# Kernel tuning notes

Hardware: AMD Instinct MI355X
Metric: run time of the kernel (lower is better)

## Reference

```python
import jax, jax.numpy as jnp
import numpy as np

N, E, B, L = 32768, 524288, 64, 512  # nodes, edges, graphs, max nodes/graph
V, D, H = 10000, 256, 512            # vocab, embed_dim, hidden_dim


def gcn_conv(h, W, b, src, dst, n):
    """PyG GCNConv: add self-loops, symmetric deg normalization, scatter-sum."""
    h = h @ W  # [n, out]
    loops = jnp.arange(n)
    s = jnp.concatenate([src, loops])
    d = jnp.concatenate([dst, loops])
    deg = jax.ops.segment_sum(jnp.ones_like(d, dtype=h.dtype), d, num_segments=n)
    dinv = jnp.where(deg > 0, jax.lax.rsqrt(deg), 0.0)
    norm = dinv[s] * dinv[d]  # [E+n]
    out = jax.ops.segment_sum(h[s] * norm[:, None], d, num_segments=n)
    return out + b


def gru_seq(x, Wih, Whh, bih, bhh):
    """torch nn.GRU (1 layer, batch_first). x: [B, T, H] -> outputs [T, B, H]."""
    def step(h, x_t):
        gi = x_t @ Wih.T + bih          # [B, 3H]
        gh = h @ Whh.T + bhh            # [B, 3H]
        ir, iz, inn = jnp.split(gi, 3, axis=-1)
        hr, hz, hn = jnp.split(gh, 3, axis=-1)
        r = jax.nn.sigmoid(ir + hr)
        z = jax.nn.sigmoid(iz + hz)
        n = jnp.tanh(inn + r * hn)
        h = (1.0 - z) * n + z * h
        return h, h
    h0 = jnp.zeros((x.shape[0], Whh.shape[1]), x.dtype)
    _, outs = jax.lax.scan(step, h0, jnp.swapaxes(x, 0, 1))
    return outs  # [T, B, H]


def setup_inputs() -> dict:
    key = jax.random.key(0)
    ks = jax.random.split(key, 16)
    s = 0.05
    x = jax.random.randint(ks[0], (N,), 0, V)
    edge_index = jax.random.randint(ks[1], (2, E), 0, N)
    batch_idx = jnp.arange(N) // L  # sorted graph ids, L nodes per graph
    focal_points = jax.random.uniform(ks[2], (B, 1), jnp.float32)
    return {
        "x": x, "edge_index": edge_index, "batch_idx": batch_idx,
        "focal_points": focal_points,
        "emb": jax.random.normal(ks[3], (V, D), jnp.float32) * s,
        "W1": jax.random.normal(ks[4], (D, H), jnp.float32) * s,
        "b1": jnp.zeros((H,), jnp.float32),
        "W2": jax.random.normal(ks[5], (H, H), jnp.float32) * s,
        "b2": jnp.zeros((H,), jnp.float32),
        "Wih": jax.random.normal(ks[6], (3 * H, H), jnp.float32) * s,
        "Whh": jax.random.normal(ks[7], (3 * H, H), jnp.float32) * s,
        "bih": jnp.zeros((3 * H,), jnp.float32),
        "bhh": jnp.zeros((3 * H,), jnp.float32),
        "fc1_w": jax.random.normal(ks[8], (H + 1, H), jnp.float32) * s,
        "fc1_b": jnp.zeros((H,), jnp.float32),
        "fc2_w": jax.random.normal(ks[9], (H, 1), jnp.float32) * s,
        "fc2_b": jnp.zeros((1,), jnp.float32),
    }


def reference(x, edge_index, batch_idx, focal_points, emb, W1, b1, W2, b2,
              Wih, Whh, bih, bhh, fc1_w, fc1_b, fc2_w, fc2_b):
    src, dst = edge_index[0], edge_index[1]
    h = emb[x]  # [N, D]
    h = jax.nn.relu(gcn_conv(h, W1, b1, src, dst, N))
    h = jax.nn.relu(gcn_conv(h, W2, b2, src, dst, N))  # [N, H]

    # Ragged -> padded: scatter each node to (graph, position-within-graph)
    ones = jnp.ones((N,), h.dtype)
    counts = jax.ops.segment_sum(ones, batch_idx, num_segments=B)
    starts = jnp.cumsum(counts) - counts  # exclusive cumsum
    pos = jnp.arange(N) - starts[batch_idx].astype(jnp.int32)
    padded = jnp.zeros((B, L, H), h.dtype).at[batch_idx, pos].set(h)

    gru_out = gru_seq(padded, Wih, Whh, bih, bhh)   # [L, B, H]
    graph_emb = gru_out.mean(axis=0)                # [B, H]
    g = jnp.concatenate([graph_emb, focal_points], axis=1)  # [B, H+1]
    out = jax.nn.relu(g @ fc1_w + fc1_b)
    out = jax.nn.sigmoid(out @ fc2_w + fc2_b)       # [B, 1]
    return out
```

## Files before the change

kernel.cpp:

```cpp
#include <hip/hip_runtime.h>

#define NODES 32768
#define EDGES 524288
#define BGR   64
#define LSEQ  512
#define DEMB  256
#define HDIM  512

typedef unsigned short u16;
typedef unsigned int   u32;
typedef unsigned long long u64;
typedef __attribute__((ext_vector_type(8))) short short8;
typedef __attribute__((ext_vector_type(4))) float f32x4;

__device__ __forceinline__ float bf2f(u16 u){ u32 x = ((u32)u)<<16; float f; __builtin_memcpy(&f,&x,4); return f; }
__device__ __forceinline__ u16 f2bf(float f){ u32 x; __builtin_memcpy(&x,&f,4); u32 r = x + 0x7fffu + ((x>>16)&1u); return (u16)(r>>16); }
__device__ __forceinline__ float lo16(u32 u){ u32 x = u<<16; float f; __builtin_memcpy(&f,&x,4); return f; }
__device__ __forceinline__ float hi16(u32 u){ u32 x = u & 0xffff0000u; float f; __builtin_memcpy(&f,&x,4); return f; }
__device__ __forceinline__ u32 pack2(float a, float b){ return (u32)f2bf(a) | ((u32)f2bf(b)<<16); }


__global__ void zero_i32(int* p, int n){
  int i = blockIdx.x*256 + threadIdx.x;
  if (i < n) p[i] = 0;
}

__global__ void transpose_cast(const float* __restrict__ in, u16* __restrict__ out, int K, int N){
  int i = blockIdx.x*256 + threadIdx.x;
  if (i < N*K){ int n = i / K, k = i - n*K; out[i] = f2bf(in[(size_t)k*N + n]); }
}

__global__ void cast_bf(const float* __restrict__ in, u16* __restrict__ out, int n){
  int i = blockIdx.x*256 + threadIdx.x;
  if (i < n) out[i] = f2bf(in[i]);
}

__global__ void count_indeg(const int* __restrict__ dst, int* __restrict__ indeg){
  int e = blockIdx.x*256 + threadIdx.x;
  if (e < EDGES) atomicAdd(&indeg[dst[e]], 1);
}

__global__ void compute_dinv(const int* __restrict__ indeg, float* __restrict__ dinv){
  int i = blockIdx.x*256 + threadIdx.x;
  if (i < NODES) dinv[i] = rsqrtf((float)(indeg[i] + 1));
}

__global__ __launch_bounds__(1024) void scan_csr(const int* __restrict__ indeg,
                                                 int* __restrict__ row_ptr,
                                                 int* __restrict__ cursor){
  __shared__ int part[1024];
  int tid = threadIdx.x, base = tid*32;
  int loc[32]; int s = 0;
  for (int i=0;i<32;i++){ loc[i] = s; s += indeg[base+i]; }
  part[tid] = s; __syncthreads();
  for (int off=1; off<1024; off<<=1){
    int v = part[tid]; int add = (tid>=off) ? part[tid-off] : 0;
    __syncthreads(); part[tid] = v + add; __syncthreads();
  }
  int offt = (tid==0) ? 0 : part[tid-1];
  for (int i=0;i<32;i++){ int v = offt + loc[i]; row_ptr[base+i] = v; cursor[base+i] = v; }
}

__global__ void fill_csr(const int* __restrict__ src, const int* __restrict__ dst,
                         int* __restrict__ cursor, int* __restrict__ csr_src){
  int e = blockIdx.x*256 + threadIdx.x;
  if (e < EDGES){ int d = dst[e]; int p = atomicAdd(&cursor[d], 1); csr_src[p] = src[e]; }
}

__global__ __launch_bounds__(256) void agg_emb(const int* __restrict__ x, const u16* __restrict__ embb,
    const float* __restrict__ dinv, const int* __restrict__ row_ptr, const int* __restrict__ indeg,
    const int* __restrict__ csr_src, u16* __restrict__ out){
  int node = blockIdx.x*4 + (threadIdx.x>>6);
  int lane = threadIdx.x & 63;
  float di = dinv[node];
  int xi = x[node];
  u64 hv = *(const u64*)(embb + (size_t)xi*DEMB + lane*4);
  u32 h0 = (u32)hv, h1 = (u32)(hv>>32);
  float a0 = lo16(h0)*di, a1 = hi16(h0)*di, a2 = lo16(h1)*di, a3 = hi16(h1)*di;
  int st = row_ptr[node], cn = indeg[node];
  for (int p = st; p < st+cn; p++){
    int s = csr_src[p];
    float ws = dinv[s];
    u64 v = *(const u64*)(embb + (size_t)x[s]*DEMB + lane*4);
    u32 w0 = (u32)v, w1 = (u32)(v>>32);
    a0 += lo16(w0)*ws; a1 += hi16(w0)*ws; a2 += lo16(w1)*ws; a3 += hi16(w1)*ws;
  }
  u64 pv = (u64)pack2(a0*di,a1*di) | ((u64)pack2(a2*di,a3*di)<<32);
  *(u64*)(out + (size_t)node*DEMB + lane*4) = pv;
}

__global__ __launch_bounds__(256) void agg_h(const u16* __restrict__ hin, const float* __restrict__ dinv,
    const int* __restrict__ row_ptr, const int* __restrict__ indeg,
    const int* __restrict__ csr_src, u16* __restrict__ out){
  int node = blockIdx.x*4 + (threadIdx.x>>6);
  int lane = threadIdx.x & 63;
  float di = dinv[node];
  float a[8];
  uint4 hv = *((const uint4*)(hin + (size_t)node*HDIM) + lane);
  a[0]=lo16(hv.x)*di; a[1]=hi16(hv.x)*di; a[2]=lo16(hv.y)*di; a[3]=hi16(hv.y)*di;
  a[4]=lo16(hv.z)*di; a[5]=hi16(hv.z)*di; a[6]=lo16(hv.w)*di; a[7]=hi16(hv.w)*di;
  int st = row_ptr[node], cn = indeg[node];
  for (int p = st; p < st+cn; p++){
    int s = csr_src[p];
    float ws = dinv[s];
    uint4 v = *((const uint4*)(hin + (size_t)s*HDIM) + lane);
    a[0]+=lo16(v.x)*ws; a[1]+=hi16(v.x)*ws; a[2]+=lo16(v.y)*ws; a[3]+=hi16(v.y)*ws;
    a[4]+=lo16(v.z)*ws; a[5]+=hi16(v.z)*ws; a[6]+=lo16(v.w)*ws; a[7]+=hi16(v.w)*ws;
  }
  uint4 o; o.x=pack2(a[0]*di,a[1]*di); o.y=pack2(a[2]*di,a[3]*di);
  o.z=pack2(a[4]*di,a[5]*di); o.w=pack2(a[6]*di,a[7]*di);
  *(uint4*)(out + (size_t)node*HDIM + lane*8) = o;
}

#define BM 128
#define BN 128
#define BKK 32
__global__ __launch_bounds__(256) void gemm_bt(const u16* __restrict__ A, const u16* __restrict__ BT,
    const float* __restrict__ bias, u16* __restrict__ C, int M, int N, int K, int relu){
  __shared__ u16 aS[BM][BKK+8];
  __shared__ u16 bS[BN][BKK+8];
  int tid = threadIdx.x;
  int m0 = blockIdx.y * BM, n0 = blockIdx.x * BN;
  int lane = tid & 63, w = tid >> 6;
  int wm = w >> 1, wn = w & 1;
  f32x4 acc[4][4];
  for (int i=0;i<4;i++) for (int j=0;j<4;j++) acc[i][j] = (f32x4)0.0f;

  int r  = tid >> 1;
  int cc = (tid & 1) * 16;
  const u16* Ag = A + (size_t)(m0 + r) * K + cc;
  const u16* Bg = BT + (size_t)(n0 + r) * K + cc;
  int l15 = lane & 15, q8 = (lane >> 4) * 8;

  for (int k0 = 0; k0 < K; k0 += BKK) {
    uint4 av0 = *(const uint4*)(Ag + k0);
    uint4 av1 = *(const uint4*)(Ag + k0 + 8);
    uint4 bv0 = *(const uint4*)(Bg + k0);
    uint4 bv1 = *(const uint4*)(Bg + k0 + 8);
    *(uint4*)&aS[r][cc]   = av0; *(uint4*)&aS[r][cc+8] = av1;
    *(uint4*)&bS[r][cc]   = bv0; *(uint4*)&bS[r][cc+8] = bv1;
    __syncthreads();
    short8 af[4], bfr[4];
    for (int i=0;i<4;i++) af[i]  = *(const short8*)&aS[wm*64 + i*16 + l15][q8];
    for (int j=0;j<4;j++) bfr[j] = *(const short8*)&bS[wn*64 + j*16 + l15][q8];
    for (int i=0;i<4;i++)
      for (int j=0;j<4;j++)
        acc[i][j] = __builtin_amdgcn_mfma_f32_16x16x32_bf16(af[i], bfr[j], acc[i][j], 0, 0, 0);
    __syncthreads();
  }
  int q = lane >> 4;
  for (int i=0;i<4;i++) for (int j=0;j<4;j++){
    int col = n0 + wn*64 + j*16 + l15;
    float bval = bias[col];
    for (int rr=0; rr<4; rr++){
      int row = m0 + wm*64 + i*16 + q*4 + rr;
      float v = acc[i][j][rr] + bval;
      if (relu) v = fmaxf(v, 0.f);
      C[(size_t)row * N + col] = f2bf(v);
    }
  }
}

__global__ __launch_bounds__(512) void gru_kernel(const u16* __restrict__ gi,
    const float* __restrict__ Whh, const float* __restrict__ bhh,
    float* __restrict__ graph_emb, u64* __restrict__ xbuf){
  __shared__ __align__(16) u16 w_swz[6*16*65*8];
  __shared__ __align__(16) u16 h_swz[2][16*65*8];
  __shared__ float gh_lds[16*100];

  int tid = threadIdx.x;
  int g = blockIdx.x >> 4, j = blockIdx.x & 15;
  int lane = tid & 63, wave = tid >> 6;
  int l15 = lane & 15, qr = (lane>>4)*4;

  for (int s = tid; s < 6144; s += 512){
    int w = s >> 10, rem = s & 1023, kc = rem >> 6, l = rem & 63;
    int row = l & 15, qq = l >> 4;
    int gate = w >> 1, half = w & 1;
    int c = gate*512 + j*32 + half*16 + row;
    const float* srcp = Whh + (size_t)c*512 + kc*32 + qq*8;
    u16* dst = w_swz + ((size_t)(w*16 + kc)*65 + l)*8;
    #pragma unroll
    for (int i2 = 0; i2 < 8; i2++) dst[i2] = f2bf(srcp[i2]);
  }
  for (int i2 = tid; i2 < 16*65*8; i2 += 512) h_swz[0][i2] = 0;

  int b = tid >> 5, hh = tid & 31;
  int bg = g*16 + b;
  int c_r = j*32 + hh, c_z = 512 + j*32 + hh, c_n = 1024 + j*32 + hh;
  float bias_r = bhh[c_r], bias_z = bhh[c_z], bias_n = bhh[c_n];
  const u16* gi_row = gi + (size_t)bg * LSEQ * 1536;
  float h_prev = 0.f, accm = 0.f;

  u64* xb = xbuf + (size_t)g * 8192;

  u16 gr0 = gi_row[c_r], gz0 = gi_row[c_z], gn0 = gi_row[c_n];
  const u16* gp1 = gi_row + 1536;
  u16 gr1 = gp1[c_r], gz1 = gp1[c_z], gn1 = gp1[c_n];

  int kcc = hh >> 1, qa = (hh & 1) * 2;
  int cb0 = (kcc*65 + (qa  )*16 + b) * 4;
  int cb1 = (kcc*65 + (qa+1)*16 + b) * 4;

  __syncthreads();

  for (int t = 0; t < LSEQ; t++){
    int tn = (t + 2 < LSEQ) ? t + 2 : t;
    const u16* gp2 = gi_row + (size_t)tn * 1536;
    u16 nr = gp2[c_r], nz = gp2[c_z], nn2 = gp2[c_n];

    if (wave < 6){
      const u16* hb = h_swz[t & 1];
      const u16* wb = w_swz + (size_t)wave*16*65*8;
      f32x4 acc0 = (f32x4)0.0f, acc1 = (f32x4)0.0f;
      #pragma unroll
      for (int kc = 0; kc < 8; kc++){
        acc0 = __builtin_amdgcn_mfma_f32_16x16x32_bf16(
                 *(const short8*)(hb + ((size_t)kc*65 + lane)*8),
                 *(const short8*)(wb + ((size_t)kc*65 + lane)*8), acc0, 0, 0, 0);
        acc1 = __builtin_amdgcn_mfma_f32_16x16x32_bf16(
                 *(const short8*)(hb + ((size_t)(kc+8)*65 + lane)*8),
                 *(const short8*)(wb + ((size_t)(kc+8)*65 + lane)*8), acc1, 0, 0, 0);
      }
      f32x4 acc = acc0 + acc1;
      int col = wave*16 + l15;
      #pragma unroll
      for (int rr2 = 0; rr2 < 4; rr2++) gh_lds[(qr + rr2)*100 + col] = acc[rr2];
    }
    __syncthreads();

    float ghr = gh_lds[b*100 + hh]      + bias_r;
    float ghz = gh_lds[b*100 + 32 + hh] + bias_z;
    float ghn = gh_lds[b*100 + 64 + hh] + bias_n;
    float rg = 1.f / (1.f + __expf(-(bf2f(gr0) + ghr)));
    float zg = 1.f / (1.f + __expf(-(bf2f(gz0) + ghz)));
    float pre = bf2f(gn0) + rg * ghn;
    pre = fminf(fmaxf(pre, -20.f), 20.f);
    float e2 = __expf(2.f * pre);
    float nn = (e2 - 1.f) / (e2 + 1.f);
    float h_new = (1.f - zg) * nn + zg * h_prev;
    accm += h_new; h_prev = h_new;

    u32 tag = (u32)(t + 1);
    float h_nb = __shfl_xor(h_new, 1, 64);
    if ((hh & 1) == 0){
      u64 val = ((u64)tag << 32) | (u64)pack2(h_new, h_nb);
      __hip_atomic_store(xb + (size_t)((t&1)*16 + b)*256 + j*16 + (hh>>1), val,
                         __ATOMIC_RELAXED, __HIP_MEMORY_SCOPE_AGENT);
    }

    const u64* rp = xb + (size_t)((t&1)*16 + b)*256 + hh*8;
    u64 v[8];
    bool ok;
    do {
      #pragma unroll
      for (int i=0;i<8;i++) v[i] = __hip_atomic_load(rp + i, __ATOMIC_RELAXED, __HIP_MEMORY_SCOPE_AGENT);
      ok = true;
      #pragma unroll
      for (int i=0;i<8;i++) ok = ok && ((u32)(v[i] >> 32) == tag);
    } while (!ok);

    u32* hl = (u32*)h_swz[(t+1) & 1];
    uint4 w0; w0.x = (u32)v[0]; w0.y = (u32)v[1]; w0.z = (u32)v[2]; w0.w = (u32)v[3];
    uint4 w1; w1.x = (u32)v[4]; w1.y = (u32)v[5]; w1.z = (u32)v[6]; w1.w = (u32)v[7];
    *(uint4*)(hl + cb0) = w0;
    *(uint4*)(hl + cb1) = w1;
    __syncthreads();

    gr0 = gr1; gz0 = gz1; gn0 = gn1;
    gr1 = nr;  gz1 = nz;  gn1 = nn2;
  }
  graph_emb[(size_t)bg*512 + j*32 + hh] = accm * (1.f/512.f);
}

__global__ __launch_bounds__(256) void head(const float* __restrict__ graph_emb, const float* __restrict__ focal,
    const float* __restrict__ fc1w, const float* __restrict__ fc1b,
    const float* __restrict__ fc2w, const float* __restrict__ fc2b, float* __restrict__ out){
  __shared__ float gv[513];
  __shared__ float h1s[512];
  __shared__ float red[4];
  int bq = blockIdx.x, tid = threadIdx.x;
  for (int i = tid; i < 512; i += 256) gv[i] = graph_emb[(size_t)bq*512 + i];
  if (tid == 0) gv[512] = focal[bq];
  __syncthreads();
  for (int c = tid; c < 512; c += 256){
    float acc = fc1b[c];
    for (int k = 0; k < 513; k++) acc += gv[k] * fc1w[(size_t)k*512 + c];
    h1s[c] = fmaxf(acc, 0.f);
  }
  __syncthreads();
  float p = h1s[tid]*fc2w[tid] + h1s[tid+256]*fc2w[tid+256];
  for (int off = 32; off; off >>= 1) p += __shfl_down(p, off, 64);
  if ((tid & 63) == 0) red[tid >> 6] = p;
  __syncthreads();
  if (tid == 0){
    float s = red[0]+red[1]+red[2]+red[3] + fc2b[0];
    out[bq] = 1.f / (1.f + __expf(-s));
  }
}

extern "C" void kernel_launch(void* const* d_in, const int* in_sizes, int n_in,
                              void* d_out, int out_size, void* d_ws, size_t ws_size,
                              hipStream_t stream){
  const int*   x     = (const int*)d_in[0];
  const int*   edge  = (const int*)d_in[1];
  const int*   srcp  = edge;
  const int*   dstp  = edge + EDGES;
  const float* focal = (const float*)d_in[3];
  const float* emb   = (const float*)d_in[4];
  const float* W1    = (const float*)d_in[5];
  const float* b1    = (const float*)d_in[6];
  const float* W2    = (const float*)d_in[7];
  const float* b2    = (const float*)d_in[8];
  const float* Wih   = (const float*)d_in[9];
  const float* Whh   = (const float*)d_in[10];
  const float* bih   = (const float*)d_in[11];
  const float* bhh   = (const float*)d_in[12];
  const float* fc1w  = (const float*)d_in[13];
  const float* fc1b  = (const float*)d_in[14];
  const float* fc2w  = (const float*)d_in[15];
  const float* fc2b  = (const float*)d_in[16];

  char* ws = (char*)d_ws;
  constexpr size_t H2_OFF    = 0;
  constexpr size_t AGG1_OFF  = 33554432;
  constexpr size_t H1_OFF    = 50331648;
  constexpr size_t AGG2_OFF  = 83886080;
  constexpr size_t GI_OFF    = 33554432;
  constexpr size_t MISC      = 134217728;
  constexpr size_t INDEG_OFF = MISC;
  constexpr size_t DINV_OFF  = MISC + 131328;
  constexpr size_t ROWPTR_OFF= MISC + 262400;
  constexpr size_t CURSOR_OFF= MISC + 393472;
  constexpr size_t CSR_OFF   = MISC + 524544;
  constexpr size_t W1T_OFF   = MISC + 2621696;
  constexpr size_t W2T_OFF   = MISC + 2883840;
  constexpr size_t WIHB_OFF  = MISC + 3408128;
  constexpr size_t XBUF_OFF  = MISC + 4980992;
  constexpr size_t GEMB_OFF  = MISC + 5243136;

  int*   indeg  = (int*)(ws + INDEG_OFF);
  float* dinv   = (float*)(ws + DINV_OFF);
  int*   rowptr = (int*)(ws + ROWPTR_OFF);
  int*   cursor = (int*)(ws + CURSOR_OFF);
  int*   csrsrc = (int*)(ws + CSR_OFF);
  u16*   W1T    = (u16*)(ws + W1T_OFF);
  u16*   W2T    = (u16*)(ws + W2T_OFF);
  u16*   WihB   = (u16*)(ws + WIHB_OFF);
  u16*   agg1   = (u16*)(ws + AGG1_OFF);
  u16*   h1     = (u16*)(ws + H1_OFF);
  u16*   agg2   = (u16*)(ws + AGG2_OFF);
  u16*   embb   = (u16*)(ws + AGG2_OFF);
  u16*   h2     = (u16*)(ws + H2_OFF);
  u16*   gi     = (u16*)(ws + GI_OFF);
  u64*   xbuf   = (u64*)(ws + XBUF_OFF);
  float* gemb   = (float*)(ws + GEMB_OFF);

  zero_i32<<<129, 256, 0, stream>>>(indeg, 32768 + 64);
  transpose_cast<<<512, 256, 0, stream>>>(W1, W1T, 256, 512);
  transpose_cast<<<1024, 256, 0, stream>>>(W2, W2T, 512, 512);
  cast_bf<<<3072, 256, 0, stream>>>(Wih, WihB, 1536*512);
  cast_bf<<<10000, 256, 0, stream>>>(emb, embb, 10000*256);
  count_indeg<<<2048, 256, 0, stream>>>(dstp, indeg);
  compute_dinv<<<128, 256, 0, stream>>>(indeg, dinv);
  scan_csr<<<1, 1024, 0, stream>>>(indeg, rowptr, cursor);
  fill_csr<<<2048, 256, 0, stream>>>(srcp, dstp, cursor, csrsrc);
  agg_emb<<<8192, 256, 0, stream>>>(x, embb, dinv, rowptr, indeg, csrsrc, agg1);
  gemm_bt<<<dim3(4, 256), 256, 0, stream>>>(agg1, W1T, b1, h1, NODES, 512, 256, 1);
  agg_h<<<8192, 256, 0, stream>>>(h1, dinv, rowptr, indeg, csrsrc, agg2);
  gemm_bt<<<dim3(4, 256), 256, 0, stream>>>(agg2, W2T, b2, h2, NODES, 512, 512, 1);
  gemm_bt<<<dim3(12, 256), 256, 0, stream>>>(h2, WihB, bih, gi, NODES, 1536, 512, 0);
  gru_kernel<<<64, 512, 0, stream>>>(gi, Whh, bhh, gemb, xbuf);
  head<<<64, 256, 0, stream>>>(gemb, focal, fc1w, fc1b, fc2w, fc2b, (float*)d_out);
}
```

Before: 2.729 ms.

## Replace tagged-payload polling with per-block flag barrier in GRU exchange

The cross-block hidden-state exchange in the GRU kernel used to pack a step tag beside each bf16 pair in 64-bit words, and every thread spun until all eight words it read carried the current tag. Now payloads are plain 32-bit stores. After a vmcnt wait and a block barrier, each block publishes one flag per step, one wave polls the 16 flags of its group, and then all threads read the payload once. This halves exchange traffic and cuts the polling to 16 flags per block instead of every thread. In exchange it adds two extra __syncthreads per step, and it relies on relaxed atomics plus s_waitcnt for ordering, with no explicit release/acquire fence, which may be fragile.

```diff
diff --git a/kernel.cpp b/kernel.cpp
--- a/kernel.cpp
+++ b/kernel.cpp
@@ -163,7 +163,7 @@
 
 __global__ __launch_bounds__(512) void gru_kernel(const u16* __restrict__ gi,
     const float* __restrict__ Whh, const float* __restrict__ bhh,
-    float* __restrict__ graph_emb, u64* __restrict__ xbuf){
+    float* __restrict__ graph_emb, u32* __restrict__ xpay, u32* __restrict__ flg){
   __shared__ __align__(16) u16 w_swz[6*16*65*8];
   __shared__ __align__(16) u16 h_swz[2][16*65*8];
   __shared__ float gh_lds[16*100];
@@ -191,8 +191,6 @@
   float bias_r = bhh[c_r], bias_z = bhh[c_z], bias_n = bhh[c_n];
   const u16* gi_row = gi + (size_t)bg * LSEQ * 1536;
   float h_prev = 0.f, accm = 0.f;
-
-  u64* xb = xbuf + (size_t)g * 8192;
 
   u16 gr0 = gi_row[c_r], gz0 = gi_row[c_z], gn0 = gi_row[c_n];
   const u16* gp1 = gi_row + 1536;
@@ -242,27 +240,40 @@
     accm += h_new; h_prev = h_new;
 
     u32 tag = (u32)(t + 1);
+    int par = t & 1;
+
     float h_nb = __shfl_xor(h_new, 1, 64);
     if ((hh & 1) == 0){
-      u64 val = ((u64)tag << 32) | (u64)pack2(h_new, h_nb);
-      __hip_atomic_store(xb + (size_t)((t&1)*16 + b)*256 + j*16 + (hh>>1), val,
+      u32 pv = pack2(h_new, h_nb);
+      __hip_atomic_store(xpay + (size_t)((g*2 + par)*16 + b)*256 + j*16 + (hh>>1), pv,
                          __ATOMIC_RELAXED, __HIP_MEMORY_SCOPE_AGENT);
     }
-
-    const u64* rp = xb + (size_t)((t&1)*16 + b)*256 + hh*8;
-    u64 v[8];
-    bool ok;
-    do {
-      #pragma unroll
-      for (int i=0;i<8;i++) v[i] = __hip_atomic_load(rp + i, __ATOMIC_RELAXED, __HIP_MEMORY_SCOPE_AGENT);
-      ok = true;
-      #pragma unroll
-      for (int i=0;i<8;i++) ok = ok && ((u32)(v[i] >> 32) == tag);
-    } while (!ok);
+    asm volatile("s_waitcnt vmcnt(0)" ::: "memory");
+    __syncthreads();
+    if (tid == 0)
+      __hip_atomic_store(flg + (g*2 + par)*16 + j, tag,
+                         __ATOMIC_RELAXED, __HIP_MEMORY_SCOPE_AGENT);
+
+    if (tid < 64){
+      const u32* fp = flg + (g*2 + par)*16;
+      bool ok;
+      do {
+        u32 f = (lane < 16)
+              ? __hip_atomic_load(fp + lane, __ATOMIC_RELAXED, __HIP_MEMORY_SCOPE_AGENT)
+              : tag;
+        ok = (f == tag);
+      } while (__ballot(ok) != 0xFFFFFFFFFFFFFFFFull);
+    }
+    __syncthreads();
+
+    const u32* rp = xpay + (size_t)((g*2 + par)*16 + b)*256 + hh*8;
+    u32 v[8];
+    #pragma unroll
+    for (int i=0;i<8;i++) v[i] = __hip_atomic_load(rp + i, __ATOMIC_RELAXED, __HIP_MEMORY_SCOPE_AGENT);
 
     u32* hl = (u32*)h_swz[(t+1) & 1];
-    uint4 w0; w0.x = (u32)v[0]; w0.y = (u32)v[1]; w0.z = (u32)v[2]; w0.w = (u32)v[3];
-    uint4 w1; w1.x = (u32)v[4]; w1.y = (u32)v[5]; w1.z = (u32)v[6]; w1.w = (u32)v[7];
+    uint4 w0; w0.x = v[0]; w0.y = v[1]; w0.z = v[2]; w0.w = v[3];
+    uint4 w1; w1.x = v[4]; w1.y = v[5]; w1.z = v[6]; w1.w = v[7];
     *(uint4*)(hl + cb0) = w0;
     *(uint4*)(hl + cb1) = w1;
     __syncthreads();
@@ -336,7 +347,8 @@
   constexpr size_t W1T_OFF   = MISC + 2621696;
   constexpr size_t W2T_OFF   = MISC + 2883840;
   constexpr size_t WIHB_OFF  = MISC + 3408128;
-  constexpr size_t XBUF_OFF  = MISC + 4980992;
+  constexpr size_t XPAY_OFF  = MISC + 4980992;
+  constexpr size_t FLG_OFF   = MISC + 5112064;
   constexpr size_t GEMB_OFF  = MISC + 5243136;
 
   int*   indeg  = (int*)(ws + INDEG_OFF);
@@ -353,7 +365,8 @@
   u16*   embb   = (u16*)(ws + AGG2_OFF);
   u16*   h2     = (u16*)(ws + H2_OFF);
   u16*   gi     = (u16*)(ws + GI_OFF);
-  u64*   xbuf   = (u64*)(ws + XBUF_OFF);
+  u32*   xpay   = (u32*)(ws + XPAY_OFF);
+  u32*   flg    = (u32*)(ws + FLG_OFF);
   float* gemb   = (float*)(ws + GEMB_OFF);
 
   zero_i32<<<129, 256, 0, stream>>>(indeg, 32768 + 64);
@@ -370,6 +383,6 @@
   agg_h<<<8192, 256, 0, stream>>>(h1, dinv, rowptr, indeg, csrsrc, agg2);
   gemm_bt<<<dim3(4, 256), 256, 0, stream>>>(agg2, W2T, b2, h2, NODES, 512, 512, 1);
   gemm_bt<<<dim3(12, 256), 256, 0, stream>>>(h2, WihB, bih, gi, NODES, 1536, 512, 0);
-  gru_kernel<<<64, 512, 0, stream>>>(gi, Whh, bhh, gemb, xbuf);
+  gru_kernel<<<64, 512, 0, stream>>>(gi, Whh, bhh, gemb, xpay, flg);
   head<<<64, 256, 0, stream>>>(gemb, focal, fc1w, fc1b, fc2w, fc2b, (float*)d_out);
 }
```

Measured after the change: 2.721 ms. No clear change (-0.3%).

## Interleave two graph groups per GRU block to hide cross-block exchange latency

Applied to the files above, without the earlier changes.

Each GRU workgroup now processes two independent 16-graph groups in alternation. Group B's MFMA and gate math run while group A's hidden-state exchange through global memory is in flight, and the reverse. The grid shrinks from 64 to 32 blocks, the gi prefetch-two-steps-ahead is replaced by direct loads each step, and each block does twice the serial work per step. The intent is to hide spin-wait and atomic latency, at the cost of fewer CUs and extra barriers per step.

```diff
diff --git a/kernel.cpp b/kernel.cpp
--- a/kernel.cpp
+++ b/kernel.cpp
@@ -166,10 +166,11 @@
     float* __restrict__ graph_emb, u64* __restrict__ xbuf){
   __shared__ __align__(16) u16 w_swz[6*16*65*8];
   __shared__ __align__(16) u16 h_swz[2][16*65*8];
-  __shared__ float gh_lds[16*100];
+  __shared__ float gh_lds[2][16*100];
 
   int tid = threadIdx.x;
-  int g = blockIdx.x >> 4, j = blockIdx.x & 15;
+  int G2 = blockIdx.x >> 4, j = blockIdx.x & 15;
+  int gA = G2*2, gB = gA + 1;
   int lane = tid & 63, wave = tid >> 6;
   int l15 = lane & 15, qr = (lane>>4)*4;
 
@@ -183,20 +184,16 @@
     #pragma unroll
     for (int i2 = 0; i2 < 8; i2++) dst[i2] = f2bf(srcp[i2]);
   }
-  for (int i2 = tid; i2 < 16*65*8; i2 += 512) h_swz[0][i2] = 0;
+  for (int i2 = tid; i2 < 2*16*65*8; i2 += 512) ((u16*)h_swz)[i2] = 0;
 
   int b = tid >> 5, hh = tid & 31;
-  int bg = g*16 + b;
   int c_r = j*32 + hh, c_z = 512 + j*32 + hh, c_n = 1024 + j*32 + hh;
   float bias_r = bhh[c_r], bias_z = bhh[c_z], bias_n = bhh[c_n];
-  const u16* gi_row = gi + (size_t)bg * LSEQ * 1536;
-  float h_prev = 0.f, accm = 0.f;
-
-  u64* xb = xbuf + (size_t)g * 8192;
-
-  u16 gr0 = gi_row[c_r], gz0 = gi_row[c_z], gn0 = gi_row[c_n];
-  const u16* gp1 = gi_row + 1536;
-  u16 gr1 = gp1[c_r], gz1 = gp1[c_z], gn1 = gp1[c_n];
+  const u16* giA = gi + (size_t)(gA*16 + b) * LSEQ * 1536;
+  const u16* giB = gi + (size_t)(gB*16 + b) * LSEQ * 1536;
+  float hpA = 0.f, hpB = 0.f, amA = 0.f, amB = 0.f;
+  u64* xbA = xbuf + (size_t)gA * 8192;
+  u64* xbB = xbuf + (size_t)gB * 8192;
 
   int kcc = hh >> 1, qa = (hh & 1) * 2;
   int cb0 = (kcc*65 + (qa  )*16 + b) * 4;
@@ -205,12 +202,55 @@
   __syncthreads();
 
   for (int t = 0; t < LSEQ; t++){
-    int tn = (t + 2 < LSEQ) ? t + 2 : t;
-    const u16* gp2 = gi_row + (size_t)tn * 1536;
-    u16 nr = gp2[c_r], nz = gp2[c_z], nn2 = gp2[c_n];
+    u32 tag = (u32)(t + 1);
+    int par = t & 1;
+
+    const u16* pA = giA + (size_t)t * 1536;
+    const u16* pB = giB + (size_t)t * 1536;
+    u16 arA = pA[c_r], azA = pA[c_z], anA = pA[c_n];
+    u16 arB = pB[c_r], azB = pB[c_z], anB = pB[c_n];
 
     if (wave < 6){
-      const u16* hb = h_swz[t & 1];
+      const u16* hb = h_swz[0];
+      const u16* wb = w_swz + (size_t)wave*16*65*8;
+      f32x4 acc0 = (f32x4)0.0f, acc1 = (f32x4)0.0f;
+      #pragma unroll
+      for (int kc = 0; kc < 8; kc++){
+        acc0 = __builtin_amdgcn_mfma_f32_16x16x32_bf16(
+                 *(const short8*)(hb + ((size_t)kc*65 + lane)*8),
+                 *(const short8*)(w_swz + ((size_t)(wave*16 + kc)*65 + lane)*8), acc0, 0, 0, 0);
+        acc1 = __builtin_amdgcn_mfma_f32_16x16x32_bf16(
+                 *(const short8*)(hb + ((size_t)(kc+8)*65 + lane)*8),
+                 *(const short8*)(wb + ((size_t)(kc+8)*65 + lane)*8), acc1, 0, 0, 0);
+      }
+      f32x4 acc = acc0 + acc1;
+      int col = wave*16 + l15;
+      #pragma unroll
+      for (int rr2 = 0; rr2 < 4; rr2++) gh_lds[0][(qr + rr2)*100 + col] = acc[rr2];
+    }
+    __syncthreads();
+
+    {
+      float ghr = gh_lds[0][b*100 + hh]      + bias_r;
+      float ghz = gh_lds[0][b*100 + 32 + hh] + bias_z;
+      float ghn = gh_lds[0][b*100 + 64 + hh] + bias_n;
+      float rg = 1.f / (1.f + __expf(-(bf2f(arA) + ghr)));
+      float zg = 1.f / (1.f + __expf(-(bf2f(azA) + ghz)));
+      float pre = bf2f(anA) + rg * ghn;
+      pre = fminf(fmaxf(pre, -20.f), 20.f);
+      float e2 = __expf(2.f * pre);
+      float nn = (e2 - 1.f) / (e2 + 1.f);
+      float h_new = (1.f - zg) * nn + zg * hpA;
+      amA += h_new; hpA = h_new;
+      float h_nb = __shfl_xor(h_new, 1, 64);
+      if ((hh & 1) == 0){
+        u64 val = ((u64)tag << 32) | (u64)pack2(h_new, h_nb);
+        __hip_atomic_store(xbA + (size_t)(par*16 + b)*256 + j*16 + (hh>>1), val,
+                           __ATOMIC_RELAXED, __HIP_MEMORY_SCOPE_AGENT);
+      }
+    }
+    if (wave < 6){
+      const u16* hb = h_swz[1];
       const u16* wb = w_swz + (size_t)wave*16*65*8;
       f32x4 acc0 = (f32x4)0.0f, acc1 = (f32x4)0.0f;
       #pragma unroll
@@ -225,52 +265,67 @@
       f32x4 acc = acc0 + acc1;
       int col = wave*16 + l15;
       #pragma unroll
-      for (int rr2 = 0; rr2 < 4; rr2++) gh_lds[(qr + rr2)*100 + col] = acc[rr2];
-    }
-    __syncthreads();
-
-    float ghr = gh_lds[b*100 + hh]      + bias_r;
-    float ghz = gh_lds[b*100 + 32 + hh] + bias_z;
-    float ghn = gh_lds[b*100 + 64 + hh] + bias_n;
-    float rg = 1.f / (1.f + __expf(-(bf2f(gr0) + ghr)));
-    float zg = 1.f / (1.f + __expf(-(bf2f(gz0) + ghz)));
-    float pre = bf2f(gn0) + rg * ghn;
-    pre = fminf(fmaxf(pre, -20.f), 20.f);
-    float e2 = __expf(2.f * pre);
-    float nn = (e2 - 1.f) / (e2 + 1.f);
-    float h_new = (1.f - zg) * nn + zg * h_prev;
-    accm += h_new; h_prev = h_new;
-
-    u32 tag = (u32)(t + 1);
-    float h_nb = __shfl_xor(h_new, 1, 64);
-    if ((hh & 1) == 0){
-      u64 val = ((u64)tag << 32) | (u64)pack2(h_new, h_nb);
-      __hip_atomic_store(xb + (size_t)((t&1)*16 + b)*256 + j*16 + (hh>>1), val,
-                         __ATOMIC_RELAXED, __HIP_MEMORY_SCOPE_AGENT);
-    }
-
-    const u64* rp = xb + (size_t)((t&1)*16 + b)*256 + hh*8;
-    u64 v[8];
-    bool ok;
-    do {
-      #pragma unroll
-      for (int i=0;i<8;i++) v[i] = __hip_atomic_load(rp + i, __ATOMIC_RELAXED, __HIP_MEMORY_SCOPE_AGENT);
-      ok = true;
-      #pragma unroll
-      for (int i=0;i<8;i++) ok = ok && ((u32)(v[i] >> 32) == tag);
-    } while (!ok);
-
-    u32* hl = (u32*)h_swz[(t+1) & 1];
-    uint4 w0; w0.x = (u32)v[0]; w0.y = (u32)v[1]; w0.z = (u32)v[2]; w0.w = (u32)v[3];
-    uint4 w1; w1.x = (u32)v[4]; w1.y = (u32)v[5]; w1.z = (u32)v[6]; w1.w = (u32)v[7];
-    *(uint4*)(hl + cb0) = w0;
-    *(uint4*)(hl + cb1) = w1;
-    __syncthreads();
-
-    gr0 = gr1; gz0 = gz1; gn0 = gn1;
-    gr1 = nr;  gz1 = nz;  gn1 = nn2;
-  }
-  graph_emb[(size_t)bg*512 + j*32 + hh] = accm * (1.f/512.f);
+      for (int rr2 = 0; rr2 < 4; rr2++) gh_lds[1][(qr + rr2)*100 + col] = acc[rr2];
+    }
+    __syncthreads();
+
+    {
+      float ghr = gh_lds[1][b*100 + hh]      + bias_r;
+      float ghz = gh_lds[1][b*100 + 32 + hh] + bias_z;
+      float ghn = gh_lds[1][b*100 + 64 + hh] + bias_n;
+      float rg = 1.f / (1.f + __expf(-(bf2f(arB) + ghr)));
+      float zg = 1.f / (1.f + __expf(-(bf2f(azB) + ghz)));
+      float pre = bf2f(anB) + rg * ghn;
+      pre = fminf(fmaxf(pre, -20.f), 20.f);
+      float e2 = __expf(2.f * pre);
+      float nn = (e2 - 1.f) / (e2 + 1.f);
+      float h_new = (1.f - zg) * nn + zg * hpB;
+      amB += h_new; hpB = h_new;
+      float h_nb = __shfl_xor(h_new, 1, 64);
+      if ((hh & 1) == 0){
+        u64 val = ((u64)tag << 32) | (u64)pack2(h_new, h_nb);
+        __hip_atomic_store(xbB + (size_t)(par*16 + b)*256 + j*16 + (hh>>1), val,
+                           __ATOMIC_RELAXED, __HIP_MEMORY_SCOPE_AGENT);
+      }
+    }
+    {
+      const u64* rp = xbA + (size_t)(par*16 + b)*256 + hh*8;
+      u64 v[8]; bool ok;
+      do {
+        #pragma unroll
+        for (int i=0;i<8;i++) v[i] = __hip_atomic_load(rp + i, __ATOMIC_RELAXED, __HIP_MEMORY_SCOPE_AGENT);
+        ok = true;
+        #pragma unroll
+        for (int i=0;i<8;i++) ok = ok && ((u32)(v[i] >> 32) == tag);
+      } while (!ok);
+      u32* hl = (u32*)h_swz[0];
+      uint4 w0; w0.x=(u32)v[0]; w0.y=(u32)v[1]; w0.z=(u32)v[2]; w0.w=(u32)v[3];
+      uint4 w1; w1.x=(u32)v[4]; w1.y=(u32)v[5]; w1.z=(u32)v[6]; w1.w=(u32)v[7];
+      *(uint4*)(hl + cb0) = w0;
+      *(uint4*)(hl + cb1) = w1;
+    }
+    __syncthreads();
+
+    {
+      const u64* rp = xbB + (size_t)(par*16 + b)*256 + hh*8;
+      u64 v[8]; bool ok;
+      do {
+        #pragma unroll
+        for (int i=0;i<8;i++) v[i] = __hip_atomic_load(rp + i, __ATOMIC_RELAXED, __HIP_MEMORY_SCOPE_AGENT);
+        ok = true;
+        #pragma unroll
+        for (int i=0;i<8;i++) ok = ok && ((u32)(v[i] >> 32) == tag);
+      } while (!ok);
+      u32* hl = (u32*)h_swz[1];
+      uint4 w0; w0.x=(u32)v[0]; w0.y=(u32)v[1]; w0.z=(u32)v[2]; w0.w=(u32)v[3];
+      uint4 w1; w1.x=(u32)v[4]; w1.y=(u32)v[5]; w1.z=(u32)v[6]; w1.w=(u32)v[7];
+      *(uint4*)(hl + cb0) = w0;
+      *(uint4*)(hl + cb1) = w1;
+    }
+    __syncthreads();
+  }
+  graph_emb[(size_t)(gA*16 + b)*512 + j*32 + hh] = amA * (1.f/512.f);
+  graph_emb[(size_t)(gB*16 + b)*512 + j*32 + hh] = amB * (1.f/512.f);
 }
 
 __global__ __launch_bounds__(256) void head(const float* __restrict__ graph_emb, const float* __restrict__ focal,
@@ -370,6 +425,6 @@
   agg_h<<<8192, 256, 0, stream>>>(h1, dinv, rowptr, indeg, csrsrc, agg2);
   gemm_bt<<<dim3(4, 256), 256, 0, stream>>>(agg2, W2T, b2, h2, NODES, 512, 512, 1);
   gemm_bt<<<dim3(12, 256), 256, 0, stream>>>(h2, WihB, bih, gi, NODES, 1536, 512, 0);
-  gru_kernel<<<64, 512, 0, stream>>>(gi, Whh, bhh, gemb, xbuf);
+  gru_kernel<<<32, 512, 0, stream>>>(gi, Whh, bhh, gemb, xbuf);
   head<<<64, 256, 0, stream>>>(gemb, focal, fc1w, fc1b, fc2w, fc2b, (float*)d_out);
 }
```

Measured after the change: 3.380 ms. +23.8%, slower.
